# Performance work log

Measured on AMD Instinct MI355X. Metric: run time of the kernel, lower is better.

Reference implementation:

```python
import jax, jax.numpy as jnp
import numpy as np

HID = 64
NP_, NE_, NF_ = 200000, 100000, 50000
E = 500000
B = 64
LN_EPS = 1e-5


def _mlp(x, w1, b1, w2, b2):
    return jax.nn.relu(x @ w1 + b1) @ w2 + b2


def _sage(x_src, x_dst, ei, Wl, bl, Wr):
    # PyG SAGEConv: out = lin_l(mean_j x_src[j]) + lin_r(x_dst); bias on lin_l.
    n = x_dst.shape[0]
    msg = x_src[ei[0]]                                   # (E, H) gather
    s = jax.ops.segment_sum(msg, ei[1], num_segments=n)  # scatter-sum
    c = jax.ops.segment_sum(jnp.ones((ei.shape[1],), x_src.dtype), ei[1], num_segments=n)
    mean = s / jnp.clip(c, 1.0)[:, None]
    return mean @ Wl + bl + x_dst @ Wr


def _ln(x, g, b):
    m = jnp.mean(x, -1, keepdims=True)
    v = jnp.mean((x - m) ** 2, -1, keepdims=True)
    return (x - m) * jax.lax.rsqrt(v + LN_EPS) * g + b


def _pool(h, batch):
    s = jax.ops.segment_sum(h, batch, num_segments=B)
    c = jax.ops.segment_sum(jnp.ones((h.shape[0],), h.dtype), batch, num_segments=B)
    return s / jnp.clip(c, 1.0)[:, None]


def setup_inputs() -> dict:
    key = jax.random.key(0)
    ks = jax.random.split(key, 40)
    d = {}
    d['point_x'] = jax.random.normal(ks[0], (NP_, 3), jnp.float32)
    d['edge_x'] = jax.random.normal(ks[1], (NE_, 2), jnp.float32)
    d['face_x'] = jax.random.normal(ks[2], (NF_, 16), jnp.float32)
    d['batch_point'] = jnp.sort(jax.random.randint(ks[3], (NP_,), 0, B, jnp.int32))
    d['batch_edge'] = jnp.sort(jax.random.randint(ks[4], (NE_,), 0, B, jnp.int32))
    d['batch_face'] = jnp.sort(jax.random.randint(ks[5], (NF_,), 0, B, jnp.int32))
    # edge_index per relation: row0 = src idx, row1 = dst idx
    def ei(k, n_src, n_dst):
        k1, k2 = jax.random.split(k)
        return jnp.stack([jax.random.randint(k1, (E,), 0, n_src, jnp.int32),
                          jax.random.randint(k2, (E,), 0, n_dst, jnp.int32)])
    d['ei_pp'] = ei(ks[6], NP_, NP_)
    d['ei_fp'] = ei(ks[7], NF_, NP_)
    d['ei_ep'] = ei(ks[8], NE_, NP_)
    d['ei_pf'] = ei(ks[9], NP_, NF_)
    d['ei_ef'] = ei(ks[10], NE_, NF_)
    d['ei_ff'] = ei(ks[11], NF_, NF_)
    d['ei_pe'] = ei(ks[12], NP_, NE_)
    d['ei_fe'] = ei(ks[13], NF_, NE_)
    s = 0.1
    d['pw1'] = jax.random.normal(ks[14], (3, HID), jnp.float32) * s
    d['pb1'] = jax.random.normal(ks[15], (HID,), jnp.float32) * s
    d['pw2'] = jax.random.normal(ks[16], (HID, HID), jnp.float32) * s
    d['pb2'] = jax.random.normal(ks[17], (HID,), jnp.float32) * s
    d['ew1'] = jax.random.normal(ks[18], (2, HID), jnp.float32) * s
    d['eb1'] = jax.random.normal(ks[19], (HID,), jnp.float32) * s
    d['ew2'] = jax.random.normal(ks[20], (HID, HID), jnp.float32) * s
    d['eb2'] = jax.random.normal(ks[21], (HID,), jnp.float32) * s
    d['fw1'] = jax.random.normal(ks[22], (16, HID), jnp.float32) * s
    d['fb1'] = jax.random.normal(ks[23], (HID,), jnp.float32) * s
    d['fw2'] = jax.random.normal(ks[24], (HID, HID), jnp.float32) * s
    d['fb2'] = jax.random.normal(ks[25], (HID,), jnp.float32) * s
    d['Wl'] = jax.random.normal(ks[26], (2, 8, HID, HID), jnp.float32) * s
    d['bl'] = jax.random.normal(ks[27], (2, 8, HID), jnp.float32) * s
    d['Wr'] = jax.random.normal(ks[28], (2, 8, HID, HID), jnp.float32) * s
    d['ln_g'] = jnp.ones((2, 3, HID), jnp.float32) + 0.1 * jax.random.normal(ks[29], (2, 3, HID), jnp.float32)
    d['ln_b'] = jax.random.normal(ks[30], (2, 3, HID), jnp.float32) * s
    return d


def reference(point_x, edge_x, face_x, batch_point, batch_edge, batch_face,
              ei_pp, ei_fp, ei_ep, ei_pf, ei_ef, ei_ff, ei_pe, ei_fe,
              pw1, pb1, pw2, pb2, ew1, eb1, ew2, eb2, fw1, fb1, fw2, fb2,
              Wl, bl, Wr, ln_g, ln_b):
    hp = _mlp(point_x, pw1, pb1, pw2, pb2)
    he = _mlp(edge_x, ew1, eb1, ew2, eb2)
    hf = _mlp(face_x, fw1, fb1, fw2, fb2)
    for i in range(2):
        # relation order: pp, fp, ep, pf, ef, ff, pe, fe ; HeteroConv aggr='sum'
        op = (_sage(hp, hp, ei_pp, Wl[i, 0], bl[i, 0], Wr[i, 0])
              + _sage(hf, hp, ei_fp, Wl[i, 1], bl[i, 1], Wr[i, 1])
              + _sage(he, hp, ei_ep, Wl[i, 2], bl[i, 2], Wr[i, 2]))
        of = (_sage(hp, hf, ei_pf, Wl[i, 3], bl[i, 3], Wr[i, 3])
              + _sage(he, hf, ei_ef, Wl[i, 4], bl[i, 4], Wr[i, 4])
              + _sage(hf, hf, ei_ff, Wl[i, 5], bl[i, 5], Wr[i, 5]))
        oe = (_sage(hp, he, ei_pe, Wl[i, 6], bl[i, 6], Wr[i, 6])
              + _sage(hf, he, ei_fe, Wl[i, 7], bl[i, 7], Wr[i, 7]))
        hp = _ln(hp + jax.nn.relu(op), ln_g[i, 0], ln_b[i, 0])
        he = _ln(he + jax.nn.relu(oe), ln_g[i, 1], ln_b[i, 1])
        hf = _ln(hf + jax.nn.relu(of), ln_g[i, 2], ln_b[i, 2])
    return jnp.concatenate([_pool(hp, batch_point), _pool(he, batch_edge), _pool(hf, batch_face)], axis=-1)
```

## Files before the change

### kernel.cpp

```cpp
#include <hip/hip_runtime.h>
#include <hip/hip_bf16.h>


#define POOL_SPLIT 4
#define NBUCK 49
#define ABLK 4096

typedef __attribute__((ext_vector_type(8))) short bf8_t;
typedef __attribute__((ext_vector_type(4))) float f32x4;

__device__ __forceinline__ ushort f2bf(float f) {
  union { __hip_bfloat16 b; ushort u; } v;
  v.b = __float2bfloat16(f);
  return v.u;
}
__device__ __forceinline__ float u2f(ushort u) {
  union { ushort u; __hip_bfloat16 b; } v;
  v.u = u;
  return __bfloat162float(v.b);
}

__global__ __launch_bounds__(256) void prep_kernel(
    const float* __restrict__ Wl, const float* __restrict__ Wr,
    const float* __restrict__ bl, const float* __restrict__ w2p,
    const float* __restrict__ w2e, const float* __restrict__ w2f,
    ushort* __restrict__ fw, float* __restrict__ bls) {
  int idx = blockIdx.x * blockDim.x + threadIdx.x;
  if (idx < 25 * 4096) {
    int m = idx >> 12, e = idx & 4095;
    int i8 = e >> 3, b = e & 7;
    int lane = i8 & 63, cb = i8 >> 6;
    int ks = cb & 1, ct = cb >> 1;
    int k = ks * 32 + ((lane >> 4) << 3) + b;
    int col = (ct << 4) + (lane & 15);
    int widx = (k << 6) + col;
    float v;
    if (m < 16) {
      v = Wl[(size_t)m * 4096 + widx];
    } else if (m < 22) {
      int c = m - 16, i = c / 3, t = c % 3;
      int rb = (t == 0) ? 0 : ((t == 1) ? 6 : 3);
      int rc = (t == 1) ? 2 : 3;
      v = 0.f;
      for (int r = 0; r < rc; ++r) v += Wr[(size_t)(i * 8 + rb + r) * 4096 + widx];
    } else {
      const float* w2 = (m == 22) ? w2p : ((m == 23) ? w2e : w2f);
      v = w2[widx];
    }
    fw[idx] = f2bf(v);
  } else if (idx < 25 * 4096 + 6 * 64) {
    int j = idx - 25 * 4096;
    int c = j >> 6, e = j & 63;
    int i = c / 3, t = c % 3;
    int rb = (t == 0) ? 0 : ((t == 1) ? 6 : 3);
    int rc = (t == 1) ? 2 : 3;
    float s = 0.f;
    for (int r = 0; r < rc; ++r) s += bl[(i * 8 + rb + r) * 64 + e];
    bls[c * 64 + e] = s;
  }
}

struct GJob { const ushort* A; const ushort* W; const float* bias; ushort* C; int n; };
struct GJobs12 { GJob j[12]; };

__device__ __forceinline__ GJob gsel(const GJobs12& js, int y) {
  switch (y) {
    case 0: return js.j[0];  case 1: return js.j[1];  case 2: return js.j[2];
    case 3: return js.j[3];  case 4: return js.j[4];  case 5: return js.j[5];
    case 6: return js.j[6];  case 7: return js.j[7];  case 8: return js.j[8];
    case 9: return js.j[9];  case 10: return js.j[10]; default: return js.j[11];
  }
}

__global__ __launch_bounds__(256) void gemm_multi_kernel(GJobs12 js) {
  GJob jb = gsel(js, blockIdx.y);
  const int n = jb.n;
  const int lane = threadIdx.x & 63;
  const int wid = (blockIdx.x * blockDim.x + threadIdx.x) >> 6;
  const int r0 = wid * 32;
  if (r0 >= n) return;
  bf8_t bw[8];
#pragma unroll
  for (int i = 0; i < 8; ++i)
    bw[i] = *(const bf8_t*)(jb.W + ((i << 6) + lane) * 8);
  const int koff = ((lane >> 4) << 3);
  int ra = r0 + (lane & 15);
  int rb = ra + 16;
  ra = min(ra, n - 1);
  rb = min(rb, n - 1);
  const bf8_t a00 = *(const bf8_t*)(jb.A + (size_t)ra * 64 + koff);
  const bf8_t a01 = *(const bf8_t*)(jb.A + (size_t)ra * 64 + 32 + koff);
  const bf8_t a10 = *(const bf8_t*)(jb.A + (size_t)rb * 64 + koff);
  const bf8_t a11 = *(const bf8_t*)(jb.A + (size_t)rb * 64 + 32 + koff);
  f32x4 acc[8];
#pragma unroll
  for (int i = 0; i < 8; ++i) acc[i] = (f32x4){0.f, 0.f, 0.f, 0.f};
#pragma unroll
  for (int ct = 0; ct < 4; ++ct) {
    acc[ct]     = __builtin_amdgcn_mfma_f32_16x16x32_bf16(a00, bw[ct * 2 + 0], acc[ct], 0, 0, 0);
    acc[ct]     = __builtin_amdgcn_mfma_f32_16x16x32_bf16(a01, bw[ct * 2 + 1], acc[ct], 0, 0, 0);
    acc[4 + ct] = __builtin_amdgcn_mfma_f32_16x16x32_bf16(a10, bw[ct * 2 + 0], acc[4 + ct], 0, 0, 0);
    acc[4 + ct] = __builtin_amdgcn_mfma_f32_16x16x32_bf16(a11, bw[ct * 2 + 1], acc[4 + ct], 0, 0, 0);
  }
  float bv[4] = {0.f, 0.f, 0.f, 0.f};
  if (jb.bias) {
#pragma unroll
    for (int ct = 0; ct < 4; ++ct) bv[ct] = jb.bias[ct * 16 + (lane & 15)];
  }
  const int rowb = r0 + ((lane >> 4) << 2);
  const int cb = lane & 15;
#pragma unroll
  for (int rt = 0; rt < 2; ++rt) {
#pragma unroll
    for (int q = 0; q < 4; ++q) {
      int row = rowb + rt * 16 + q;
      if (row < n) {
#pragma unroll
        for (int ct = 0; ct < 4; ++ct)
          jb.C[(size_t)row * 64 + ct * 16 + cb] = f2bf(acc[rt * 4 + ct][q] + bv[ct]);
      }
    }
  }
}

template <int FIN>
__device__ __forceinline__ void mlp1_body(
    const float* __restrict__ x, const float* __restrict__ w1,
    const float* __restrict__ b1, ushort* __restrict__ h1, int n) {
  const int lane = threadIdx.x & 63;
  int wid = (blockIdx.x * blockDim.x + threadIdx.x) >> 6;
  const int nw = (gridDim.x * blockDim.x) >> 6;
  float w1c[FIN];
#pragma unroll
  for (int k = 0; k < FIN; ++k) w1c[k] = w1[k * 64 + lane];
  const float b1v = b1[lane];
  for (int r = wid; r < n; r += nw) {
    float s = b1v;
#pragma unroll
    for (int k = 0; k < FIN; ++k) s = fmaf(x[(size_t)r * FIN + k], w1c[k], s);
    h1[(size_t)r * 64 + lane] = f2bf(fmaxf(s, 0.f));
  }
}

struct MLPJob { const float* x; const float* w1; const float* b1; ushort* o; int n; };
struct MLPack { MLPJob j[3]; };

__global__ __launch_bounds__(256) void mlp1_kernel(MLPack a) {
  if (blockIdx.y == 0)      mlp1_body<3>(a.j[0].x, a.j[0].w1, a.j[0].b1, a.j[0].o, a.j[0].n);
  else if (blockIdx.y == 1) mlp1_body<2>(a.j[1].x, a.j[1].w1, a.j[1].b1, a.j[1].o, a.j[1].n);
  else                      mlp1_body<16>(a.j[2].x, a.j[2].w1, a.j[2].b1, a.j[2].o, a.j[2].n);
}

struct EIPack {
  const int* e0; const int* e1; const int* e2; const int* e3;
  const int* e4; const int* e5; const int* e6; const int* e7;
  int b0, b1, b2, b3, b4, b5, b6, b7;
};

__device__ __forceinline__ void ei_sel(const EIPack& t, int r, const int*& ei, int& b) {
  switch (r) {
    case 0: ei = t.e0; b = t.b0; break;
    case 1: ei = t.e1; b = t.b1; break;
    case 2: ei = t.e2; b = t.b2; break;
    case 3: ei = t.e3; b = t.b3; break;
    case 4: ei = t.e4; b = t.b4; break;
    case 5: ei = t.e5; b = t.b5; break;
    case 6: ei = t.e6; b = t.b6; break;
    default: ei = t.e7; b = t.b7; break;
  }
}

__device__ __forceinline__ int rel_shift(int rel) {
  return rel < 3 ? 12 : (rel < 6 ? 10 : 11);
}

__global__ __launch_bounds__(256) void binA1_kernel(EIPack t, int* __restrict__ counts,
                                                    int E, int nblk) {
  __shared__ int hist[NBUCK];
  int rel = blockIdx.x % 8, blk = blockIdx.x / 8;
  const int* ei; int bb;
  ei_sel(t, rel, ei, bb);
  int shift = rel_shift(rel);
  for (int i = threadIdx.x; i < NBUCK; i += 256) hist[i] = 0;
  __syncthreads();
  int e0 = blk * ABLK;
  for (int i = threadIdx.x; i < ABLK; i += 256) {
    int e = e0 + i;
    if (e < E) {
      int d = __builtin_nontemporal_load(ei + E + e);
      atomicAdd(&hist[d >> shift], 1);
    }
  }
  __syncthreads();
  for (int i = threadIdx.x; i < NBUCK; i += 256)
    counts[(rel * NBUCK + i) * nblk + blk] = hist[i];
}

__global__ __launch_bounds__(256) void binA2_kernel(EIPack t, const int* __restrict__ coff,
                                                    int* __restrict__ bed,
                                                    int E, int nblk) {
  __shared__ int cur[NBUCK];
  int rel = blockIdx.x % 8, blk = blockIdx.x / 8;
  const int* ei; int bb;
  ei_sel(t, rel, ei, bb);
  int shift = rel_shift(rel);
  int lmask = (1 << shift) - 1;
  for (int i = threadIdx.x; i < NBUCK; i += 256)
    cur[i] = coff[(rel * NBUCK + i) * nblk + blk];
  __syncthreads();
  int e0 = blk * ABLK;
  for (int i = threadIdx.x; i < ABLK; i += 256) {
    int e = e0 + i;
    if (e < E) {
      int s = __builtin_nontemporal_load(ei + e);
      int d = __builtin_nontemporal_load(ei + E + e);
      int p = atomicAdd(&cur[d >> shift], 1);
      bed[p] = ((d & lmask) << 18) | s;
    }
  }
}

__global__ __launch_bounds__(256) void binB_kernel(const int* __restrict__ coff,
                                                   const int* __restrict__ bed,
                                                   int* __restrict__ off,
                                                   int* __restrict__ srcs,
                                                   int nblk, int NP_, int NF_, int NE_,
                                                   int Etot) {
  __shared__ int hist[4096];
  __shared__ int wsum[4];
  int gb = blockIdx.x;
  int rel = gb / NBUCK, b = gb % NBUCK;
  int shift = rel_shift(rel);
  int D = 1 << shift;
  int ndst_r = rel < 3 ? NP_ : (rel < 6 ? NF_ : NE_);
  int rbase = rel < 3 ? rel * NP_
            : (rel < 6 ? 3 * NP_ + (rel - 3) * NF_
                       : 3 * NP_ + 3 * NF_ + (rel - 6) * NE_);
  int d0 = b << shift;
  int Dl = min(D, ndst_r - d0);
  int ebase = coff[gb * nblk];
  int eend  = coff[(gb + 1) * nblk];
  for (int i = threadIdx.x; i < D; i += 256) hist[i] = 0;
  __syncthreads();
  for (int e = ebase + threadIdx.x; e < eend; e += 256)
    atomicAdd(&hist[bed[e] >> 18], 1);
  __syncthreads();
  const int PT = D >> 8;
  int tbase = threadIdx.x * PT;
  int ts = 0;
  for (int k = 0; k < PT; ++k) ts += hist[tbase + k];
  int lane = threadIdx.x & 63, w = threadIdx.x >> 6;
  int x = ts;
#pragma unroll
  for (int dd = 1; dd < 64; dd <<= 1) {
    int y = __shfl_up(x, dd, 64);
    if (lane >= dd) x += y;
  }
  if (lane == 63) wsum[w] = x;
  __syncthreads();
  int woff = 0;
#pragma unroll
  for (int k = 0; k < 4; ++k)
    if (k < w) woff += wsum[k];
  int pos = woff + x - ts;
  for (int k = 0; k < PT; ++k) {
    int c = hist[tbase + k];
    hist[tbase + k] = pos;
    if (tbase + k < Dl) off[rbase + d0 + tbase + k] = ebase + pos;
    pos += c;
  }
  __syncthreads();
  for (int e = ebase + threadIdx.x; e < eend; e += 256) {
    int w_ = bed[e];
    int p = atomicAdd(&hist[w_ >> 18], 1);
    srcs[ebase + p] = w_ & 0x3FFFF;
  }
  if (gb == 0 && threadIdx.x == 0)
    off[3 * NP_ + 3 * NF_ + 2 * NE_] = Etot;
}

__global__ __launch_bounds__(256) void scan1_kernel(const int* __restrict__ cnt,
                                                    int* __restrict__ part, int n) {
  __shared__ int wt[4];
  int base = blockIdx.x * 1024;
  int t = 0;
  for (int i = threadIdx.x; i < 1024; i += 256) {
    int idx = base + i;
    if (idx < n) t += cnt[idx];
  }
#pragma unroll
  for (int d = 32; d > 0; d >>= 1) t += __shfl_xor(t, d, 64);
  if ((threadIdx.x & 63) == 0) wt[threadIdx.x >> 6] = t;
  __syncthreads();
  if (threadIdx.x == 0) part[blockIdx.x] = wt[0] + wt[1] + wt[2] + wt[3];
}

__global__ __launch_bounds__(1024) void scan2_kernel(int* __restrict__ part,
                                                     int* __restrict__ off, int nb,
                                                     int n, int total) {
  __shared__ int lds[1024];
  int tid = threadIdx.x;
  int v = (tid < nb) ? part[tid] : 0;
  lds[tid] = v;
  __syncthreads();
  for (int d = 1; d < 1024; d <<= 1) {
    int y = (tid >= d) ? lds[tid - d] : 0;
    __syncthreads();
    lds[tid] += y;
    __syncthreads();
  }
  if (tid < nb) part[tid] = lds[tid] - v;
  if (tid == 0) off[n] = total;
}

__global__ __launch_bounds__(256) void scan3_kernel(const int* cnt,
                                                    const int* __restrict__ part,
                                                    int* __restrict__ out, int n) {
  __shared__ int wt[4];
  int base = blockIdx.x * 1024 + threadIdx.x * 4;
  int c[4];
#pragma unroll
  for (int k = 0; k < 4; ++k) {
    int idx = base + k;
    c[k] = (idx < n) ? cnt[idx] : 0;
  }
  int t = c[0] + c[1] + c[2] + c[3];
  int lane = threadIdx.x & 63, w = threadIdx.x >> 6;
  int x = t;
#pragma unroll
  for (int d = 1; d < 64; d <<= 1) {
    int y = __shfl_up(x, d, 64);
    if (lane >= d) x += y;
  }
  int ex = x - t;
  if (lane == 63) wt[w] = x;
  __syncthreads();
  int woff = 0;
#pragma unroll
  for (int k = 0; k < 4; ++k)
    if (k < w) woff += wt[k];
  int pos = part[blockIdx.x] + woff + ex;
#pragma unroll
  for (int k = 0; k < 4; ++k) {
    int idx = base + k;
    if (idx < n) out[idx] = pos;
    pos += c[k];
  }
}

__device__ __forceinline__ void gather_rel(const ushort* __restrict__ g,
    const int* __restrict__ srcs, int e0, int e1, int l8, float o[8]) {
  float t8[8];
#pragma unroll
  for (int c = 0; c < 8; ++c) t8[c] = 0.f;
  int j = e0;
  for (; j + 2 <= e1; j += 2) {
    int s0 = srcs[j], s1 = srcs[j + 1];
    bf8_t v0 = *(const bf8_t*)(g + (size_t)s0 * 64 + l8 * 8);
    bf8_t v1 = *(const bf8_t*)(g + (size_t)s1 * 64 + l8 * 8);
#pragma unroll
    for (int c = 0; c < 8; ++c) t8[c] += u2f((ushort)v0[c]) + u2f((ushort)v1[c]);
  }
  if (j < e1) {
    int s = srcs[j];
    bf8_t v = *(const bf8_t*)(g + (size_t)s * 64 + l8 * 8);
#pragma unroll
    for (int c = 0; c < 8; ++c) t8[c] += u2f((ushort)v[c]);
  }
  float inv = 1.f / fmaxf((float)(e1 - e0), 1.f);
#pragma unroll
  for (int c = 0; c < 8; ++c) o[c] = fmaf(t8[c], inv, o[c]);
}

struct GFType {
  const ushort* g0; const ushort* g1; const ushort* g2;
  const ushort* t;  ushort* h;
  const float* bls; const float* lng; const float* lnb;
  int b0, b1, b2, nrel, ndst;
};
struct GFPack { GFType t[3]; };

__global__ __launch_bounds__(256) void gf_kernel(GFPack pk, const int* __restrict__ srcs,
                                                 const int* __restrict__ off) {
  GFType ty = (blockIdx.y == 0) ? pk.t[0] : (blockIdx.y == 1) ? pk.t[1] : pk.t[2];
  const int l8 = threadIdx.x & 7;
  const int d = (blockIdx.x * blockDim.x + threadIdx.x) >> 3;
  if (d >= ty.ndst) return;
  int e0a = off[ty.b0 + d], e1a = off[ty.b0 + d + 1];
  int e0b = 0, e1b = 0, e0c = 0, e1c = 0;
  if (ty.nrel > 1) { e0b = off[ty.b1 + d]; e1b = off[ty.b1 + d + 1]; }
  if (ty.nrel > 2) { e0c = off[ty.b2 + d]; e1c = off[ty.b2 + d + 1]; }
  float blr[8], ggr[8], bbr[8];
  *(float4*)(blr)     = *(const float4*)(ty.bls + l8 * 8);
  *(float4*)(blr + 4) = *(const float4*)(ty.bls + l8 * 8 + 4);
  *(float4*)(ggr)     = *(const float4*)(ty.lng + l8 * 8);
  *(float4*)(ggr + 4) = *(const float4*)(ty.lng + l8 * 8 + 4);
  *(float4*)(bbr)     = *(const float4*)(ty.lnb + l8 * 8);
  *(float4*)(bbr + 4) = *(const float4*)(ty.lnb + l8 * 8 + 4);
  float o[8];
#pragma unroll
  for (int c = 0; c < 8; ++c) o[c] = 0.f;
  gather_rel(ty.g0, srcs, e0a, e1a, l8, o);
  if (ty.nrel > 1) gather_rel(ty.g1, srcs, e0b, e1b, l8, o);
  if (ty.nrel > 2) gather_rel(ty.g2, srcs, e0c, e1c, l8, o);
  bf8_t tv = *(const bf8_t*)(ty.t + (size_t)d * 64 + l8 * 8);
  bf8_t hv = *(const bf8_t*)(ty.h + (size_t)d * 64 + l8 * 8);
  float v[8];
  float s = 0.f;
#pragma unroll
  for (int c = 0; c < 8; ++c) {
    float x = u2f((ushort)hv[c]) + fmaxf(o[c] + u2f((ushort)tv[c]) + blr[c], 0.f);
    v[c] = x;
    s += x;
  }
  s += __shfl_xor(s, 1, 64);
  s += __shfl_xor(s, 2, 64);
  s += __shfl_xor(s, 4, 64);
  float m = s * (1.f / 64.f);
  float vs = 0.f;
#pragma unroll
  for (int c = 0; c < 8; ++c) {
    float dd = v[c] - m;
    vs += dd * dd;
  }
  vs += __shfl_xor(vs, 1, 64);
  vs += __shfl_xor(vs, 2, 64);
  vs += __shfl_xor(vs, 4, 64);
  float rstd = rsqrtf(vs * (1.f / 64.f) + 1e-5f);
  bf8_t outv;
#pragma unroll
  for (int c = 0; c < 8; ++c)
    outv[c] = (short)f2bf((v[c] - m) * rstd * ggr[c] + bbr[c]);
  *(bf8_t*)(ty.h + (size_t)d * 64 + l8 * 8) = outv;
}

struct PoolArgs {
  const ushort* h0; const ushort* h1; const ushort* h2;
  const int* b0; const int* b1; const int* b2;
  int n0, n1, n2;
};

__global__ __launch_bounds__(256) void pool_kernel(PoolArgs a, float* __restrict__ out) {
  int ty = blockIdx.y;
  const ushort* h = (ty == 0) ? a.h0 : (ty == 1) ? a.h1 : a.h2;
  const int* batch = (ty == 0) ? a.b0 : (ty == 1) ? a.b1 : a.b2;
  int n = (ty == 0) ? a.n0 : (ty == 1) ? a.n1 : a.n2;
  int col_base = ty * 64;
  int gph = blockIdx.x >> 2;
  int s = blockIdx.x & 3;
  int lo = 0, hi = n;
  while (lo < hi) { int mid = (lo + hi) >> 1; if (batch[mid] < gph) lo = mid + 1; else hi = mid; }
  int beg = lo;
  hi = n;
  while (lo < hi) { int mid = (lo + hi) >> 1; if (batch[mid] < gph + 1) lo = mid + 1; else hi = mid; }
  int end = lo;
  int cnt = end - beg;
  if (cnt <= 0) return;
  int per = (cnt + POOL_SPLIT - 1) >> 2;
  int rb = beg + s * per;
  int re = min(rb + per, end);
  if (rb >= re) return;
  const int l8 = threadIdx.x & 7;
  const int grp = threadIdx.x >> 3;
  float o[8];
#pragma unroll
  for (int c = 0; c < 8; ++c) o[c] = 0.f;
  for (int r = rb + grp; r < re; r += 32) {
    bf8_t v = *(const bf8_t*)(h + (size_t)r * 64 + l8 * 8);
#pragma unroll
    for (int c = 0; c < 8; ++c) o[c] += u2f((ushort)v[c]);
  }
#pragma unroll
  for (int c = 0; c < 8; ++c) {
    o[c] += __shfl_xor(o[c], 8, 64);
    o[c] += __shfl_xor(o[c], 16, 64);
    o[c] += __shfl_xor(o[c], 32, 64);
  }
  if ((threadIdx.x & 56) == 0) {
#pragma unroll
    for (int c = 0; c < 8; ++c)
      unsafeAtomicAdd(out + gph * 192 + col_base + l8 * 8 + c, o[c]);
  }
}

__global__ __launch_bounds__(256) void pool_scale_kernel(
    float* __restrict__ out, const int* __restrict__ bp,
    const int* __restrict__ be, const int* __restrict__ bf,
    int np, int ne, int nf) {
  int idx = blockIdx.x * blockDim.x + threadIdx.x;
  if (idx >= 64 * 192) return;
  int gph = idx / 192, col = idx % 192;
  const int* b;
  int n;
  if (col < 64) { b = bp; n = np; }
  else if (col < 128) { b = be; n = ne; }
  else { b = bf; n = nf; }
  int lo = 0, hi = n;
  while (lo < hi) { int mid = (lo + hi) >> 1; if (b[mid] < gph) lo = mid + 1; else hi = mid; }
  int beg = lo;
  hi = n;
  while (lo < hi) { int mid = (lo + hi) >> 1; if (b[mid] < gph + 1) lo = mid + 1; else hi = mid; }
  int cnt = lo - beg;
  out[idx] = out[idx] / fmaxf((float)cnt, 1.f);
}

extern "C" void kernel_launch(void* const* d_in, const int* in_sizes, int n_in,
                              void* d_out, int out_size, void* d_ws, size_t ws_size,
                              hipStream_t stream) {
  const float* point_x = (const float*)d_in[0];
  const float* edge_x  = (const float*)d_in[1];
  const float* face_x  = (const float*)d_in[2];
  const int* bp = (const int*)d_in[3];
  const int* be = (const int*)d_in[4];
  const int* bf = (const int*)d_in[5];
  const int NP = in_sizes[3], NE = in_sizes[4], NF = in_sizes[5];
  const int Eg = in_sizes[6] / 2;

  const float* Wl  = (const float*)d_in[26];
  const float* blp = (const float*)d_in[27];
  const float* Wr  = (const float*)d_in[28];
  const float* lng = (const float*)d_in[29];
  const float* lnb = (const float*)d_in[30];

  int nsrc[8] = {NP, NF, NE, NP, NE, NF, NP, NF};
  int ndst[8] = {NP, NP, NP, NF, NF, NF, NE, NE};
  int base[8], gb[8];
  base[0] = 0; gb[0] = 0;
  for (int r = 1; r < 8; ++r) {
    base[r] = base[r - 1] + ndst[r - 1];
    gb[r] = gb[r - 1] + nsrc[r - 1];
  }
  const size_t GROWS = (size_t)gb[7] + nsrc[7];
  const int NDSUM = 3 * NP + 3 * NF + 2 * NE;

  char* p = (char*)d_ws;
  ushort* hA = (ushort*)p; p += (size_t)(NP + NE + NF) * 64 * 2;
  ushort* g_all = (ushort*)p; p += GROWS * 64 * 2;
  ushort* t_all = (ushort*)p; p += (size_t)(NP + NE + NF) * 64 * 2;
  ushort* fw = (ushort*)p; p += (size_t)25 * 4096 * 2;
  float* bls = (float*)p; p += 6 * 64 * 4;
  int* srcs = (int*)p; p += (size_t)8 * Eg * 4;
  int* off = (int*)p; p += (size_t)(NDSUM + 1) * 4;
  const int nblk = (Eg + ABLK - 1) / ABLK;
  const int NCNT = 8 * NBUCK * nblk;
  int* counts = (int*)p; p += (size_t)NCNT * 4;
  int* coff = (int*)p; p += (size_t)(NCNT + 1) * 4;
  int* part = (int*)p; p += 4096;
  int* bed = (int*)g_all;

  ushort* hp_ = hA;
  ushort* he_ = hA + (size_t)NP * 64;
  ushort* hf_ = hA + (size_t)(NP + NE) * 64;
  ushort* tP = t_all;
  ushort* tE = t_all + (size_t)NP * 64;
  ushort* tF = t_all + (size_t)(NP + NE) * 64;

  const int* ei[8] = {(const int*)d_in[6],  (const int*)d_in[7],
                      (const int*)d_in[8],  (const int*)d_in[9],
                      (const int*)d_in[10], (const int*)d_in[11],
                      (const int*)d_in[12], (const int*)d_in[13]};
  EIPack ep;
  ep.e0 = ei[0]; ep.e1 = ei[1]; ep.e2 = ei[2]; ep.e3 = ei[3];
  ep.e4 = ei[4]; ep.e5 = ei[5]; ep.e6 = ei[6]; ep.e7 = ei[7];
  ep.b0 = base[0]; ep.b1 = base[1]; ep.b2 = base[2]; ep.b3 = base[3];
  ep.b4 = base[4]; ep.b5 = base[5]; ep.b6 = base[6]; ep.b7 = base[7];

  binA1_kernel<<<8 * nblk, 256, 0, stream>>>(ep, counts, Eg, nblk);
  const int nb = (NCNT + 1023) / 1024;
  scan1_kernel<<<nb, 256, 0, stream>>>(counts, part, NCNT);
  scan2_kernel<<<1, 1024, 0, stream>>>(part, coff, nb, NCNT, 8 * Eg);
  scan3_kernel<<<nb, 256, 0, stream>>>(counts, part, coff, NCNT);
  binA2_kernel<<<8 * nblk, 256, 0, stream>>>(ep, coff, bed, Eg, nblk);
  binB_kernel<<<8 * NBUCK, 256, 0, stream>>>(coff, bed, off, srcs,
                                             nblk, NP, NF, NE, 8 * Eg);

  prep_kernel<<<(25 * 4096 + 6 * 64 + 255) / 256, 256, 0, stream>>>(
      Wl, Wr, blp, (const float*)d_in[16], (const float*)d_in[20],
      (const float*)d_in[24], fw, bls);

  auto gblk = [](int n) { return ((n + 31) / 32 + 3) / 4; };

  ushort* sp = t_all;
  ushort* se = t_all + (size_t)NP * 64;
  ushort* sf = t_all + (size_t)(NP + NE) * 64;
  MLPack ma;
  ma.j[0] = {point_x, (const float*)d_in[14], (const float*)d_in[15], sp, NP};
  ma.j[1] = {edge_x,  (const float*)d_in[18], (const float*)d_in[19], se, NE};
  ma.j[2] = {face_x,  (const float*)d_in[22], (const float*)d_in[23], sf, NF};
  mlp1_kernel<<<dim3(512, 3), 256, 0, stream>>>(ma);

  GJobs12 init{};
  init.j[0] = {sp, fw + 22 * 4096, (const float*)d_in[17], hp_, NP};
  init.j[1] = {se, fw + 23 * 4096, (const float*)d_in[21], he_, NE};
  init.j[2] = {sf, fw + 24 * 4096, (const float*)d_in[25], hf_, NF};
  gemm_multi_kernel<<<dim3(gblk(NP), 3), 256, 0, stream>>>(init);

  const ushort* hsrc[8] = {hp_, hf_, he_, hp_, he_, hf_, hp_, hf_};
  const int gfx = (NP * 8 + 255) / 256;

  for (int i = 0; i < 2; ++i) {
    GJobs12 js{};
    for (int r = 0; r < 8; ++r)
      js.j[r] = {hsrc[r], fw + (size_t)(i * 8 + r) * 4096, nullptr,
                 g_all + (size_t)gb[r] * 64, nsrc[r]};
    js.j[8]  = {hp_, fw + (size_t)(16 + i * 3 + 0) * 4096, nullptr, tP, NP};
    js.j[9]  = {he_, fw + (size_t)(16 + i * 3 + 1) * 4096, nullptr, tE, NE};
    js.j[10] = {hf_, fw + (size_t)(16 + i * 3 + 2) * 4096, nullptr, tF, NF};
    gemm_multi_kernel<<<dim3(gblk(NP), 11), 256, 0, stream>>>(js);

    GFPack pk;
    pk.t[0] = {g_all + (size_t)gb[0] * 64, g_all + (size_t)gb[1] * 64,
               g_all + (size_t)gb[2] * 64, tP, hp_,
               bls + (i * 3 + 0) * 64, lng + (i * 3 + 0) * 64, lnb + (i * 3 + 0) * 64,
               base[0], base[1], base[2], 3, NP};
    pk.t[1] = {g_all + (size_t)gb[3] * 64, g_all + (size_t)gb[4] * 64,
               g_all + (size_t)gb[5] * 64, tF, hf_,
               bls + (i * 3 + 2) * 64, lng + (i * 3 + 2) * 64, lnb + (i * 3 + 2) * 64,
               base[3], base[4], base[5], 3, NF};
    pk.t[2] = {g_all + (size_t)gb[6] * 64, g_all + (size_t)gb[7] * 64,
               g_all + (size_t)gb[6] * 64, tE, he_,
               bls + (i * 3 + 1) * 64, lng + (i * 3 + 1) * 64, lnb + (i * 3 + 1) * 64,
               base[6], base[7], 0, 2, NE};
    gf_kernel<<<dim3(gfx, 3), 256, 0, stream>>>(pk, srcs, off);
  }

  float* out = (float*)d_out;
  hipMemsetAsync(out, 0, (size_t)out_size * sizeof(float), stream);
  PoolArgs pa;
  pa.h0 = hp_; pa.h1 = he_; pa.h2 = hf_;
  pa.b0 = bp; pa.b1 = be; pa.b2 = bf;
  pa.n0 = NP; pa.n1 = NE; pa.n2 = NF;
  pool_kernel<<<dim3(64 * POOL_SPLIT, 3), 256, 0, stream>>>(pa, out);
  pool_scale_kernel<<<(64 * 192 + 255) / 256, 256, 0, stream>>>(out, bp, be, bf, NP, NE, NF);
}
```

Measured before the change: 480.1 us.

## Aggregate raw features first, then fuse one K=256 GEMM with LayerNorm per node type

The old code transformed every source node with a per-relation GEMM before gathering the projected rows. The new kernel instead gathers and mean-aggregates the raw hidden features per relation into shared memory. It then runs a single stacked K=256 MFMA GEMM against a concatenated [Wl_r...; sum Wr] weight matrix, with bias, residual and LayerNorm fused into the same kernel. This removes the 11-job GEMM launch and the large intermediate g/t buffers, and ping-pongs hidden state between two buffers. The cost is an extra bf16 rounding of the aggregated means before the matmul, and more shared-memory use per block.

```diff
diff --git a/kernel.cpp b/kernel.cpp
--- a/kernel.cpp
+++ b/kernel.cpp
@@ -24,32 +24,19 @@
     const float* __restrict__ Wl, const float* __restrict__ Wr,
     const float* __restrict__ bl, const float* __restrict__ w2p,
     const float* __restrict__ w2e, const float* __restrict__ w2f,
-    ushort* __restrict__ fw, float* __restrict__ bls) {
+    ushort* __restrict__ fw0, float* __restrict__ bls, ushort* __restrict__ fws) {
   int idx = blockIdx.x * blockDim.x + threadIdx.x;
-  if (idx < 25 * 4096) {
+  if (idx < 3 * 4096) {
     int m = idx >> 12, e = idx & 4095;
     int i8 = e >> 3, b = e & 7;
     int lane = i8 & 63, cb = i8 >> 6;
     int ks = cb & 1, ct = cb >> 1;
     int k = ks * 32 + ((lane >> 4) << 3) + b;
     int col = (ct << 4) + (lane & 15);
-    int widx = (k << 6) + col;
-    float v;
-    if (m < 16) {
-      v = Wl[(size_t)m * 4096 + widx];
-    } else if (m < 22) {
-      int c = m - 16, i = c / 3, t = c % 3;
-      int rb = (t == 0) ? 0 : ((t == 1) ? 6 : 3);
-      int rc = (t == 1) ? 2 : 3;
-      v = 0.f;
-      for (int r = 0; r < rc; ++r) v += Wr[(size_t)(i * 8 + rb + r) * 4096 + widx];
-    } else {
-      const float* w2 = (m == 22) ? w2p : ((m == 23) ? w2e : w2f);
-      v = w2[widx];
-    }
-    fw[idx] = f2bf(v);
-  } else if (idx < 25 * 4096 + 6 * 64) {
-    int j = idx - 25 * 4096;
+    const float* w2 = (m == 0) ? w2p : ((m == 1) ? w2e : w2f);
+    fw0[idx] = f2bf(w2[(k << 6) + col]);
+  } else if (idx < 3 * 4096 + 6 * 64) {
+    int j = idx - 3 * 4096;
     int c = j >> 6, e = j & 63;
     int i = c / 3, t = c % 3;
     int rb = (t == 0) ? 0 : ((t == 1) ? 6 : 3);
@@ -57,23 +44,36 @@
     float s = 0.f;
     for (int r = 0; r < rc; ++r) s += bl[(i * 8 + rb + r) * 64 + e];
     bls[c * 64 + e] = s;
+  } else if (idx < 3 * 4096 + 6 * 64 + 6 * 16384) {
+    int j = idx - (3 * 4096 + 6 * 64);
+    int m = j >> 14, e = j & 16383;
+    int i = m / 3, t = m % 3;
+    int i8 = e >> 3, b = e & 7;
+    int lane = i8 & 63, cb = i8 >> 6;
+    int ct = cb >> 3, ks = cb & 7;
+    int k = ks * 32 + ((lane >> 4) << 3) + b;
+    int col = (ct << 4) + (lane & 15);
+    int rb = (t == 0) ? 0 : ((t == 1) ? 6 : 3);
+    int rc = (t == 1) ? 2 : 3;
+    float v;
+    if (k < 192) {
+      int sec = k >> 6;
+      if (sec >= rc) v = 0.f;
+      else v = Wl[(size_t)(i * 8 + rb + sec) * 4096 + ((k & 63) << 6) + col];
+    } else {
+      v = 0.f;
+      for (int r = 0; r < rc; ++r)
+        v += Wr[(size_t)(i * 8 + rb + r) * 4096 + ((k - 192) << 6) + col];
+    }
+    fws[(size_t)m * 16384 + e] = f2bf(v);
   }
 }
 
 struct GJob { const ushort* A; const ushort* W; const float* bias; ushort* C; int n; };
-struct GJobs12 { GJob j[12]; };
-
-__device__ __forceinline__ GJob gsel(const GJobs12& js, int y) {
-  switch (y) {
-    case 0: return js.j[0];  case 1: return js.j[1];  case 2: return js.j[2];
-    case 3: return js.j[3];  case 4: return js.j[4];  case 5: return js.j[5];
-    case 6: return js.j[6];  case 7: return js.j[7];  case 8: return js.j[8];
-    case 9: return js.j[9];  case 10: return js.j[10]; default: return js.j[11];
-  }
-}
-
-__global__ __launch_bounds__(256) void gemm_multi_kernel(GJobs12 js) {
-  GJob jb = gsel(js, blockIdx.y);
+struct GJobs3 { GJob j0, j1, j2; };
+
+__global__ __launch_bounds__(256) void gemm3_kernel(GJobs3 js) {
+  GJob jb = (blockIdx.y == 0) ? js.j0 : (blockIdx.y == 1) ? js.j1 : js.j2;
   const int n = jb.n;
   const int lane = threadIdx.x & 63;
   const int wid = (blockIdx.x * blockDim.x + threadIdx.x) >> 6;
@@ -102,11 +102,9 @@
     acc[4 + ct] = __builtin_amdgcn_mfma_f32_16x16x32_bf16(a10, bw[ct * 2 + 0], acc[4 + ct], 0, 0, 0);
     acc[4 + ct] = __builtin_amdgcn_mfma_f32_16x16x32_bf16(a11, bw[ct * 2 + 1], acc[4 + ct], 0, 0, 0);
   }
-  float bv[4] = {0.f, 0.f, 0.f, 0.f};
-  if (jb.bias) {
-#pragma unroll
-    for (int ct = 0; ct < 4; ++ct) bv[ct] = jb.bias[ct * 16 + (lane & 15)];
-  }
+  float bv[4];
+#pragma unroll
+  for (int ct = 0; ct < 4; ++ct) bv[ct] = jb.bias[ct * 16 + (lane & 15)];
   const int rowb = r0 + ((lane >> 4) << 2);
   const int cb = lane & 15;
 #pragma unroll
@@ -348,9 +346,17 @@
   }
 }
 
-__device__ __forceinline__ void gather_rel(const ushort* __restrict__ g,
-    const int* __restrict__ srcs, int e0, int e1, int l8, float o[8]) {
-  float t8[8];
+struct GMType {
+  const ushort* s0; const ushort* s1; const ushort* s2;
+  const ushort* hd;  ushort* hn;
+  const ushort* ws;
+  const float* bls; const float* lng; const float* lnb;
+  int b0, b1, b2, nrel, ndst;
+};
+struct GMPack { GMType t[3]; };
+
+__device__ __forceinline__ void gm_gather(const ushort* __restrict__ g,
+    const int* __restrict__ srcs, int e0, int e1, int l8, float t8[8]) {
 #pragma unroll
   for (int c = 0; c < 8; ++c) t8[c] = 0.f;
   int j = e0;
@@ -369,69 +375,112 @@
   }
   float inv = 1.f / fmaxf((float)(e1 - e0), 1.f);
 #pragma unroll
-  for (int c = 0; c < 8; ++c) o[c] = fmaf(t8[c], inv, o[c]);
-}
-
-struct GFType {
-  const ushort* g0; const ushort* g1; const ushort* g2;
-  const ushort* t;  ushort* h;
-  const float* bls; const float* lng; const float* lnb;
-  int b0, b1, b2, nrel, ndst;
-};
-struct GFPack { GFType t[3]; };
-
-__global__ __launch_bounds__(256) void gf_kernel(GFPack pk, const int* __restrict__ srcs,
-                                                 const int* __restrict__ off) {
-  GFType ty = (blockIdx.y == 0) ? pk.t[0] : (blockIdx.y == 1) ? pk.t[1] : pk.t[2];
+  for (int c = 0; c < 8; ++c) t8[c] *= inv;
+}
+
+__global__ __launch_bounds__(256) void gmm_kernel(GMPack pk, const int* __restrict__ srcs,
+                                                  const int* __restrict__ off) {
+  GMType ty = (blockIdx.y == 0) ? pk.t[0] : (blockIdx.y == 1) ? pk.t[1] : pk.t[2];
+  const int rowbase = blockIdx.x * 64;
+  if (rowbase >= ty.ndst) return;
+  __shared__ ushort Ml[64 * 256];
+
+  const int grp = threadIdx.x >> 3;
   const int l8 = threadIdx.x & 7;
-  const int d = (blockIdx.x * blockDim.x + threadIdx.x) >> 3;
-  if (d >= ty.ndst) return;
-  int e0a = off[ty.b0 + d], e1a = off[ty.b0 + d + 1];
-  int e0b = 0, e1b = 0, e0c = 0, e1c = 0;
-  if (ty.nrel > 1) { e0b = off[ty.b1 + d]; e1b = off[ty.b1 + d + 1]; }
-  if (ty.nrel > 2) { e0c = off[ty.b2 + d]; e1c = off[ty.b2 + d + 1]; }
-  float blr[8], ggr[8], bbr[8];
-  *(float4*)(blr)     = *(const float4*)(ty.bls + l8 * 8);
-  *(float4*)(blr + 4) = *(const float4*)(ty.bls + l8 * 8 + 4);
-  *(float4*)(ggr)     = *(const float4*)(ty.lng + l8 * 8);
-  *(float4*)(ggr + 4) = *(const float4*)(ty.lng + l8 * 8 + 4);
-  *(float4*)(bbr)     = *(const float4*)(ty.lnb + l8 * 8);
-  *(float4*)(bbr + 4) = *(const float4*)(ty.lnb + l8 * 8 + 4);
-  float o[8];
-#pragma unroll
-  for (int c = 0; c < 8; ++c) o[c] = 0.f;
-  gather_rel(ty.g0, srcs, e0a, e1a, l8, o);
-  if (ty.nrel > 1) gather_rel(ty.g1, srcs, e0b, e1b, l8, o);
-  if (ty.nrel > 2) gather_rel(ty.g2, srcs, e0c, e1c, l8, o);
-  bf8_t tv = *(const bf8_t*)(ty.t + (size_t)d * 64 + l8 * 8);
-  bf8_t hv = *(const bf8_t*)(ty.h + (size_t)d * 64 + l8 * 8);
-  float v[8];
-  float s = 0.f;
-#pragma unroll
-  for (int c = 0; c < 8; ++c) {
-    float x = u2f((ushort)hv[c]) + fmaxf(o[c] + u2f((ushort)tv[c]) + blr[c], 0.f);
-    v[c] = x;
-    s += x;
-  }
-  s += __shfl_xor(s, 1, 64);
-  s += __shfl_xor(s, 2, 64);
-  s += __shfl_xor(s, 4, 64);
-  float m = s * (1.f / 64.f);
-  float vs = 0.f;
-#pragma unroll
-  for (int c = 0; c < 8; ++c) {
-    float dd = v[c] - m;
-    vs += dd * dd;
-  }
-  vs += __shfl_xor(vs, 1, 64);
-  vs += __shfl_xor(vs, 2, 64);
-  vs += __shfl_xor(vs, 4, 64);
-  float rstd = rsqrtf(vs * (1.f / 64.f) + 1e-5f);
-  bf8_t outv;
-#pragma unroll
-  for (int c = 0; c < 8; ++c)
-    outv[c] = (short)f2bf((v[c] - m) * rstd * ggr[c] + bbr[c]);
-  *(bf8_t*)(ty.h + (size_t)d * 64 + l8 * 8) = outv;
+#pragma unroll
+  for (int rr = 0; rr < 2; ++rr) {
+    int lr = grp * 2 + rr;
+    int d = rowbase + lr;
+    int sw = lr & 7;
+    bf8_t zero = {};
+    if (d < ty.ndst) {
+      float t8[8];
+      bf8_t pkd;
+      gm_gather(ty.s0, srcs, off[ty.b0 + d], off[ty.b0 + d + 1], l8, t8);
+#pragma unroll
+      for (int c = 0; c < 8; ++c) pkd[c] = (short)f2bf(t8[c]);
+      *(bf8_t*)(Ml + lr * 256 + ((0 * 8 + l8) ^ sw) * 8) = pkd;
+      gm_gather(ty.s1, srcs, off[ty.b1 + d], off[ty.b1 + d + 1], l8, t8);
+#pragma unroll
+      for (int c = 0; c < 8; ++c) pkd[c] = (short)f2bf(t8[c]);
+      *(bf8_t*)(Ml + lr * 256 + ((1 * 8 + l8) ^ sw) * 8) = pkd;
+      if (ty.nrel > 2) {
+        gm_gather(ty.s2, srcs, off[ty.b2 + d], off[ty.b2 + d + 1], l8, t8);
+#pragma unroll
+        for (int c = 0; c < 8; ++c) pkd[c] = (short)f2bf(t8[c]);
+        *(bf8_t*)(Ml + lr * 256 + ((2 * 8 + l8) ^ sw) * 8) = pkd;
+      } else {
+        *(bf8_t*)(Ml + lr * 256 + ((2 * 8 + l8) ^ sw) * 8) = zero;
+      }
+      *(bf8_t*)(Ml + lr * 256 + ((3 * 8 + l8) ^ sw) * 8) =
+          *(const bf8_t*)(ty.hd + (size_t)d * 64 + l8 * 8);
+    } else {
+#pragma unroll
+      for (int s = 0; s < 4; ++s)
+        *(bf8_t*)(Ml + lr * 256 + ((s * 8 + l8) ^ sw) * 8) = zero;
+    }
+  }
+  __syncthreads();
+
+  const int lane = threadIdx.x & 63;
+  const int w = threadIdx.x >> 6;
+  const int lr = w * 16 + (lane & 15);
+  f32x4 acc[4];
+#pragma unroll
+  for (int i = 0; i < 4; ++i) acc[i] = (f32x4){0.f, 0.f, 0.f, 0.f};
+#pragma unroll
+  for (int ks = 0; ks < 8; ++ks) {
+    int c8 = ks * 4 + (lane >> 4);
+    bf8_t af = *(const bf8_t*)(Ml + lr * 256 + (c8 ^ (lr & 7)) * 8);
+#pragma unroll
+    for (int ct = 0; ct < 4; ++ct) {
+      bf8_t bf = *(const bf8_t*)(ty.ws + ((size_t)(ct * 8 + ks) * 64 + lane) * 8);
+      acc[ct] = __builtin_amdgcn_mfma_f32_16x16x32_bf16(af, bf, acc[ct], 0, 0, 0);
+    }
+  }
+
+  const int cl = lane & 15;
+  float blv[4], ggv[4], bbv[4];
+#pragma unroll
+  for (int ct = 0; ct < 4; ++ct) {
+    blv[ct] = ty.bls[ct * 16 + cl];
+    ggv[ct] = ty.lng[ct * 16 + cl];
+    bbv[ct] = ty.lnb[ct * 16 + cl];
+  }
+#pragma unroll
+  for (int q = 0; q < 4; ++q) {
+    int d = rowbase + w * 16 + ((lane >> 4) << 2) + q;
+    if (d < ty.ndst) {
+      float v[4];
+      float s = 0.f;
+#pragma unroll
+      for (int ct = 0; ct < 4; ++ct) {
+        float hv = u2f(ty.hd[(size_t)d * 64 + ct * 16 + cl]);
+        float x = hv + fmaxf(acc[ct][q] + blv[ct], 0.f);
+        v[ct] = x;
+        s += x;
+      }
+      s += __shfl_xor(s, 1, 64);
+      s += __shfl_xor(s, 2, 64);
+      s += __shfl_xor(s, 4, 64);
+      s += __shfl_xor(s, 8, 64);
+      float m = s * (1.f / 64.f);
+      float vs = 0.f;
+#pragma unroll
+      for (int ct = 0; ct < 4; ++ct) {
+        float dd = v[ct] - m;
+        vs += dd * dd;
+      }
+      vs += __shfl_xor(vs, 1, 64);
+      vs += __shfl_xor(vs, 2, 64);
+      vs += __shfl_xor(vs, 4, 64);
+      vs += __shfl_xor(vs, 8, 64);
+      float rstd = rsqrtf(vs * (1.f / 64.f) + 1e-5f);
+#pragma unroll
+      for (int ct = 0; ct < 4; ++ct)
+        ty.hn[(size_t)d * 64 + ct * 16 + cl] = f2bf((v[ct] - m) * rstd * ggv[ct] + bbv[ct]);
+    }
+  }
 }
 
 struct PoolArgs {
@@ -522,23 +571,18 @@
   const float* lng = (const float*)d_in[29];
   const float* lnb = (const float*)d_in[30];
 
-  int nsrc[8] = {NP, NF, NE, NP, NE, NF, NP, NF};
   int ndst[8] = {NP, NP, NP, NF, NF, NF, NE, NE};
-  int base[8], gb[8];
-  base[0] = 0; gb[0] = 0;
-  for (int r = 1; r < 8; ++r) {
-    base[r] = base[r - 1] + ndst[r - 1];
-    gb[r] = gb[r - 1] + nsrc[r - 1];
-  }
-  const size_t GROWS = (size_t)gb[7] + nsrc[7];
+  int base[8];
+  base[0] = 0;
+  for (int r = 1; r < 8; ++r) base[r] = base[r - 1] + ndst[r - 1];
   const int NDSUM = 3 * NP + 3 * NF + 2 * NE;
 
   char* p = (char*)d_ws;
   ushort* hA = (ushort*)p; p += (size_t)(NP + NE + NF) * 64 * 2;
-  ushort* g_all = (ushort*)p; p += GROWS * 64 * 2;
-  ushort* t_all = (ushort*)p; p += (size_t)(NP + NE + NF) * 64 * 2;
-  ushort* fw = (ushort*)p; p += (size_t)25 * 4096 * 2;
+  ushort* hB = (ushort*)p; p += (size_t)(NP + NE + NF) * 64 * 2;
+  ushort* fw0 = (ushort*)p; p += (size_t)3 * 4096 * 2;
   float* bls = (float*)p; p += 6 * 64 * 4;
+  ushort* fws = (ushort*)p; p += (size_t)6 * 16384 * 2;
   int* srcs = (int*)p; p += (size_t)8 * Eg * 4;
   int* off = (int*)p; p += (size_t)(NDSUM + 1) * 4;
   const int nblk = (Eg + ABLK - 1) / ABLK;
@@ -546,14 +590,11 @@
   int* counts = (int*)p; p += (size_t)NCNT * 4;
   int* coff = (int*)p; p += (size_t)(NCNT + 1) * 4;
   int* part = (int*)p; p += 4096;
-  int* bed = (int*)g_all;
-
-  ushort* hp_ = hA;
-  ushort* he_ = hA + (size_t)NP * 64;
-  ushort* hf_ = hA + (size_t)(NP + NE) * 64;
-  ushort* tP = t_all;
-  ushort* tE = t_all + (size_t)NP * 64;
-  ushort* tF = t_all + (size_t)(NP + NE) * 64;
+  int* bed = (int*)hB;
+
+  ushort* h_[2][3];
+  h_[0][0] = hA; h_[0][1] = hA + (size_t)NP * 64; h_[0][2] = hA + (size_t)(NP + NE) * 64;
+  h_[1][0] = hB; h_[1][1] = hB + (size_t)NP * 64; h_[1][2] = hB + (size_t)(NP + NE) * 64;
 
   const int* ei[8] = {(const int*)d_in[6],  (const int*)d_in[7],
                       (const int*)d_in[8],  (const int*)d_in[9],
@@ -574,60 +615,47 @@
   binB_kernel<<<8 * NBUCK, 256, 0, stream>>>(coff, bed, off, srcs,
                                              nblk, NP, NF, NE, 8 * Eg);
 
-  prep_kernel<<<(25 * 4096 + 6 * 64 + 255) / 256, 256, 0, stream>>>(
+  prep_kernel<<<(3 * 4096 + 6 * 64 + 6 * 16384 + 255) / 256, 256, 0, stream>>>(
       Wl, Wr, blp, (const float*)d_in[16], (const float*)d_in[20],
-      (const float*)d_in[24], fw, bls);
-
-  auto gblk = [](int n) { return ((n + 31) / 32 + 3) / 4; };
-
-  ushort* sp = t_all;
-  ushort* se = t_all + (size_t)NP * 64;
-  ushort* sf = t_all + (size_t)(NP + NE) * 64;
+      (const float*)d_in[24], fw0, bls, fws);
+
   MLPack ma;
-  ma.j[0] = {point_x, (const float*)d_in[14], (const float*)d_in[15], sp, NP};
-  ma.j[1] = {edge_x,  (const float*)d_in[18], (const float*)d_in[19], se, NE};
-  ma.j[2] = {face_x,  (const float*)d_in[22], (const float*)d_in[23], sf, NF};
+  ma.j[0] = {point_x, (const float*)d_in[14], (const float*)d_in[15], h_[1][0], NP};
+  ma.j[1] = {edge_x,  (const float*)d_in[18], (const float*)d_in[19], h_[1][1], NE};
+  ma.j[2] = {face_x,  (const float*)d_in[22], (const float*)d_in[23], h_[1][2], NF};
   mlp1_kernel<<<dim3(512, 3), 256, 0, stream>>>(ma);
 
-  GJobs12 init{};
-  init.j[0] = {sp, fw + 22 * 4096, (const float*)d_in[17], hp_, NP};
-  init.j[1] = {se, fw + 23 * 4096, (const float*)d_in[21], he_, NE};
-  init.j[2] = {sf, fw + 24 * 4096, (const float*)d_in[25], hf_, NF};
-  gemm_multi_kernel<<<dim3(gblk(NP), 3), 256, 0, stream>>>(init);
-
-  const ushort* hsrc[8] = {hp_, hf_, he_, hp_, he_, hf_, hp_, hf_};
-  const int gfx = (NP * 8 + 255) / 256;
-
+  GJobs3 init;
+  init.j0 = {h_[1][0], fw0 + 0 * 4096, (const float*)d_in[17], h_[0][0], NP};
+  init.j1 = {h_[1][1], fw0 + 1 * 4096, (const float*)d_in[21], h_[0][1], NE};
+  init.j2 = {h_[1][2], fw0 + 2 * 4096, (const float*)d_in[25], h_[0][2], NF};
+  gemm3_kernel<<<dim3(((NP + 31) / 32 + 3) / 4, 3), 256, 0, stream>>>(init);
+
+  const int gmx = (NP + 63) / 64;
+  int cs = 0;
   for (int i = 0; i < 2; ++i) {
-    GJobs12 js{};
-    for (int r = 0; r < 8; ++r)
-      js.j[r] = {hsrc[r], fw + (size_t)(i * 8 + r) * 4096, nullptr,
-                 g_all + (size_t)gb[r] * 64, nsrc[r]};
-    js.j[8]  = {hp_, fw + (size_t)(16 + i * 3 + 0) * 4096, nullptr, tP, NP};
-    js.j[9]  = {he_, fw + (size_t)(16 + i * 3 + 1) * 4096, nullptr, tE, NE};
-    js.j[10] = {hf_, fw + (size_t)(16 + i * 3 + 2) * 4096, nullptr, tF, NF};
-    gemm_multi_kernel<<<dim3(gblk(NP), 11), 256, 0, stream>>>(js);
-
-    GFPack pk;
-    pk.t[0] = {g_all + (size_t)gb[0] * 64, g_all + (size_t)gb[1] * 64,
-               g_all + (size_t)gb[2] * 64, tP, hp_,
+    int ns = cs ^ 1;
+    ushort* hp_ = h_[cs][0];
+    ushort* he_ = h_[cs][1];
+    ushort* hf_ = h_[cs][2];
+    GMPack pk;
+    pk.t[0] = {hp_, hf_, he_, hp_, h_[ns][0], fws + (size_t)(i * 3 + 0) * 16384,
                bls + (i * 3 + 0) * 64, lng + (i * 3 + 0) * 64, lnb + (i * 3 + 0) * 64,
                base[0], base[1], base[2], 3, NP};
-    pk.t[1] = {g_all + (size_t)gb[3] * 64, g_all + (size_t)gb[4] * 64,
-               g_all + (size_t)gb[5] * 64, tF, hf_,
+    pk.t[1] = {hp_, he_, hf_, hf_, h_[ns][2], fws + (size_t)(i * 3 + 2) * 16384,
                bls + (i * 3 + 2) * 64, lng + (i * 3 + 2) * 64, lnb + (i * 3 + 2) * 64,
                base[3], base[4], base[5], 3, NF};
-    pk.t[2] = {g_all + (size_t)gb[6] * 64, g_all + (size_t)gb[7] * 64,
-               g_all + (size_t)gb[6] * 64, tE, he_,
+    pk.t[2] = {hp_, hf_, nullptr, he_, h_[ns][1], fws + (size_t)(i * 3 + 1) * 16384,
                bls + (i * 3 + 1) * 64, lng + (i * 3 + 1) * 64, lnb + (i * 3 + 1) * 64,
                base[6], base[7], 0, 2, NE};
-    gf_kernel<<<dim3(gfx, 3), 256, 0, stream>>>(pk, srcs, off);
+    gmm_kernel<<<dim3(gmx, 3), 256, 0, stream>>>(pk, srcs, off);
+    cs = ns;
   }
 
   float* out = (float*)d_out;
   hipMemsetAsync(out, 0, (size_t)out_size * sizeof(float), stream);
   PoolArgs pa;
-  pa.h0 = hp_; pa.h1 = he_; pa.h2 = hf_;
+  pa.h0 = h_[cs][0]; pa.h1 = h_[cs][1]; pa.h2 = h_[cs][2];
   pa.b0 = bp; pa.b1 = be; pa.b2 = bf;
   pa.n0 = NP; pa.n1 = NE; pa.n2 = NF;
   pool_kernel<<<dim3(64 * POOL_SPLIT, 3), 256, 0, stream>>>(pa, out);
```

Measured after the change: 509.9 us. 6.2% more time.
